# Kernel optimization log

Hardware: AMD Instinct MI355X
Metric: run time of the kernel (lower is better)

## Reference

```python
import jax, jax.numpy as jnp
import numpy as np

D_K = 512  # attn_dim

def setup_inputs() -> dict:
    key = jax.random.key(0)
    ks = jax.random.split(key, 10)
    B, S, D, A, Dv = 8, 2048, 1024, 512, 512
    Q = jax.random.normal(ks[0], (B, S, D), dtype=jnp.float32)
    K = jax.random.normal(ks[1], (B, S, D), dtype=jnp.float32)
    V = jax.random.normal(ks[2], (B, S, D), dtype=jnp.float32)
    attn_mask = jax.random.randint(ks[3], (B, S, S), 0, 2, dtype=jnp.int32)
    s = 1.0 / np.sqrt(D)
    Wq = jax.random.normal(ks[4], (A, D), dtype=jnp.float32) * s
    bq = jnp.zeros((A,), dtype=jnp.float32)
    Wk = jax.random.normal(ks[5], (A, D), dtype=jnp.float32) * s
    bk = jnp.zeros((A,), dtype=jnp.float32)
    Wv = jax.random.normal(ks[6], (Dv, D), dtype=jnp.float32) * s
    bv = jnp.zeros((Dv,), dtype=jnp.float32)
    return {"Q": Q, "K": K, "V": V, "attn_mask": attn_mask,
            "Wq": Wq, "bq": bq, "Wk": Wk, "bk": bk, "Wv": Wv, "bv": bv}

def reference(Q, K, V, attn_mask, Wq, bq, Wk, bk, Wv, bv):
    # Linear projections (torch Linear: x @ W.T + b)
    Qp = jnp.einsum('bsd,ad->bsa', Q, Wq) + bq          # [B,S,A]
    Kp = jnp.einsum('bsd,ad->bsa', K, Wk) + bk          # [B,S,A]
    WV = jnp.einsum('bsd,vd->bsv', V, Wv) + bv          # [B,S,Dv]
    scale = 1.0 / np.sqrt(D_K).astype(np.float32)
    scores = jnp.einsum('bqa,bka->bqk', Qp, Kp) * scale  # [B,S,S]
    scores = scores + attn_mask.astype(scores.dtype) * (-1e9)
    scores = jnp.swapaxes(scores, -1, -2)               # transpose BEFORE softmax
    attn = jax.nn.softmax(scores, axis=-1)              # normalize over query axis
    selfOutput = jnp.einsum('bkq,bqv->bkv', attn, WV)   # [B,S,Dv]
    return selfOutput, attn
```

## Files before the change

kernel.cpp:

```cpp
#include <hip/hip_runtime.h>
#include <stdint.h>

#define B_N   8
#define S_N   2048
#define D_N   1024
#define A_N   512
#define DV_N  512

typedef __attribute__((ext_vector_type(8))) short bf16x8;
typedef __attribute__((ext_vector_type(4))) float f32x4;

__device__ __forceinline__ unsigned short f2bf(float x) {
    union { float f; unsigned int u; } v; v.f = x;
    return (unsigned short)((v.u + 0x7fffu + ((v.u >> 16) & 1u)) >> 16);
}

__global__ void cvt_f32_bf16(const float* __restrict__ src,
                             unsigned short* __restrict__ dst, int n4) {
    int i = blockIdx.x * blockDim.x + threadIdx.x;
    if (i >= n4) return;
    float4 v = ((const float4*)src)[i];
    ushort4 o;
    o.x = f2bf(v.x); o.y = f2bf(v.y); o.z = f2bf(v.z); o.w = f2bf(v.w);
    ((ushort4*)dst)[i] = o;
}

__device__ __forceinline__ void gld_lds16(const void* g, void* l) {
    __builtin_amdgcn_global_load_lds(
        (const __attribute__((address_space(1))) unsigned int*)g,
        (__attribute__((address_space(3))) unsigned int*)l, 16, 0, 0);
}

__global__ __launch_bounds__(256) void pack_maskT(const int* __restrict__ mask,
                                                  unsigned int* __restrict__ mpT) {
    __shared__ int tile[64 * 129];
    const int b  = blockIdx.z;
    const int q0 = blockIdx.y * 64;
    const int k0 = blockIdx.x * 128;
    const int tid = threadIdx.x;
    const long long base = (long long)b * S_N * S_N;
#pragma unroll
    for (int it = 0; it < 8; ++it) {
        int c = it * 256 + tid;
        int row  = c >> 5;
        int col4 = (c & 31) * 4;
        int4 v = *(const int4*)&mask[base + (long long)(q0 + row) * S_N + k0 + col4];
        int* d = &tile[row * 129 + col4];
        d[0] = v.x; d[1] = v.y; d[2] = v.z; d[3] = v.w;
    }
    __syncthreads();
    const int wave = tid >> 6, lane = tid & 63;
#pragma unroll
    for (int kk = 0; kk < 32; ++kk) {
        const int k = wave * 32 + kk;
        const int v = tile[lane * 129 + k];
        const unsigned long long bal = __ballot(v != 0);
        if (lane == 0) {
            unsigned int* o = &mpT[(long long)(b * S_N + k0 + k) * 64 + (q0 >> 5)];
            o[0] = (unsigned int)bal;
            o[1] = (unsigned int)(bal >> 32);
        }
    }
}

template <int MODE>
__global__ __launch_bounds__(256) void gemm_nt(
    const unsigned short* __restrict__ A, const unsigned short* __restrict__ B,
    void* __restrict__ C, const float* __restrict__ bias,
    int M, int N, int K,
    long long sA, long long sB, long long sC, float scale)
{
    __shared__ __align__(16) unsigned short As[128 * 32];
    __shared__ __align__(16) unsigned short Bs[128 * 32];

    const int tid  = threadIdx.x;
    const int wave = tid >> 6;
    const int lane = tid & 63;
    const int lrow = lane & 15;
    const int quad = lane >> 4;
    const int wm = wave & 1;
    const int wn = wave >> 1;
    const int b  = blockIdx.z;
    const int m0 = blockIdx.y * 128;
    const int n0 = blockIdx.x * 128;

    const unsigned short* Ab = A + (long long)b * sA;
    const unsigned short* Bb = B + (long long)b * sB;

    f32x4 acc[4][4];
#pragma unroll
    for (int i = 0; i < 4; ++i)
#pragma unroll
        for (int j = 0; j < 4; ++j) acc[i][j] = (f32x4){0.f, 0.f, 0.f, 0.f};

    const int srow = lane >> 2;
    const int scol = (lane & 3) * 8;

    for (int kt = 0; kt < K; kt += 32) {
#pragma unroll
        for (int t = 0; t < 2; ++t) {
            const int seg = t * 4 + wave;
            const unsigned short* ga =
                Ab + (long long)(m0 + seg * 16 + srow) * K + kt + scol;
            gld_lds16(ga, &As[seg * 16 * 32]);
            const unsigned short* gb =
                Bb + (long long)(n0 + seg * 16 + srow) * K + kt + scol;
            gld_lds16(gb, &Bs[seg * 16 * 32]);
        }
        __syncthreads();

        bf16x8 af[4], bfr[4];
#pragma unroll
        for (int i = 0; i < 4; ++i)
            af[i] = *(const bf16x8*)&As[(wm * 64 + i * 16 + lrow) * 32 + quad * 8];
#pragma unroll
        for (int j = 0; j < 4; ++j)
            bfr[j] = *(const bf16x8*)&Bs[(wn * 64 + j * 16 + lrow) * 32 + quad * 8];
#pragma unroll
        for (int i = 0; i < 4; ++i)
#pragma unroll
            for (int j = 0; j < 4; ++j)
                acc[i][j] = __builtin_amdgcn_mfma_f32_16x16x32_bf16(
                    af[i], bfr[j], acc[i][j], 0, 0, 0);
        __syncthreads();
    }

#pragma unroll
    for (int i = 0; i < 4; ++i) {
        const int rowb = m0 + wm * 64 + i * 16 + quad * 4;
#pragma unroll
        for (int j = 0; j < 4; ++j) {
            const int col = n0 + wn * 64 + j * 16 + lrow;
#pragma unroll
            for (int r = 0; r < 4; ++r) {
                const int row = rowb + r;
                float v = acc[i][j][r];
                if (MODE == 0) {
                    v += bias[col];
                    ((unsigned short*)C)[(long long)row * N + col] = f2bf(v);
                } else if (MODE == 1) {
                    v += bias[row];
                    (((unsigned short*)C) + (long long)b * sC)
                        [(long long)row * N + col] = f2bf(v);
                } else if (MODE == 2) {
                    v *= scale;
                    (((float*)C) + (long long)b * sC)[(long long)row * N + col] = v;
                } else {
                    (((float*)C) + (long long)b * sC)[(long long)row * N + col] = v;
                }
            }
        }
    }
}

__global__ __launch_bounds__(256) void softmax_rows(
    float* __restrict__ sT, unsigned short* __restrict__ pbf,
    const unsigned int* __restrict__ mpT)
{
    const long long row = blockIdx.x;
    float* p = sT + row * S_N;
    unsigned short* q = pbf + row * S_N;
    const int tid = threadIdx.x;
    const int wave = tid >> 6, lane = tid & 63;

    float4 v0 = ((const float4*)p)[tid];
    float4 v1 = ((const float4*)p)[tid + 256];

    const unsigned int* mp = mpT + row * 64;
    const unsigned int w0 = mp[tid >> 3];
    const unsigned int w1 = mp[32 + (tid >> 3)];
    const int sh = (tid & 7) * 4;
    v0.x += ((w0 >> (sh + 0)) & 1u) ? -1e9f : 0.0f;
    v0.y += ((w0 >> (sh + 1)) & 1u) ? -1e9f : 0.0f;
    v0.z += ((w0 >> (sh + 2)) & 1u) ? -1e9f : 0.0f;
    v0.w += ((w0 >> (sh + 3)) & 1u) ? -1e9f : 0.0f;
    v1.x += ((w1 >> (sh + 0)) & 1u) ? -1e9f : 0.0f;
    v1.y += ((w1 >> (sh + 1)) & 1u) ? -1e9f : 0.0f;
    v1.z += ((w1 >> (sh + 2)) & 1u) ? -1e9f : 0.0f;
    v1.w += ((w1 >> (sh + 3)) & 1u) ? -1e9f : 0.0f;

    float mx = fmaxf(fmaxf(fmaxf(v0.x, v0.y), fmaxf(v0.z, v0.w)),
                     fmaxf(fmaxf(v1.x, v1.y), fmaxf(v1.z, v1.w)));
#pragma unroll
    for (int off = 32; off; off >>= 1) mx = fmaxf(mx, __shfl_xor(mx, off));

    __shared__ float redm[4];
    __shared__ float reds[4];
    if (lane == 0) redm[wave] = mx;
    __syncthreads();
    mx = fmaxf(fmaxf(redm[0], redm[1]), fmaxf(redm[2], redm[3]));

    float e[8];
    e[0] = __expf(v0.x - mx); e[1] = __expf(v0.y - mx);
    e[2] = __expf(v0.z - mx); e[3] = __expf(v0.w - mx);
    e[4] = __expf(v1.x - mx); e[5] = __expf(v1.y - mx);
    e[6] = __expf(v1.z - mx); e[7] = __expf(v1.w - mx);

    float sum = e[0] + e[1] + e[2] + e[3] + e[4] + e[5] + e[6] + e[7];
#pragma unroll
    for (int off = 32; off; off >>= 1) sum += __shfl_xor(sum, off);
    if (lane == 0) reds[wave] = sum;
    __syncthreads();
    sum = reds[0] + reds[1] + reds[2] + reds[3];
    const float inv = 1.0f / sum;

    float4 o0 = {e[0] * inv, e[1] * inv, e[2] * inv, e[3] * inv};
    float4 o1 = {e[4] * inv, e[5] * inv, e[6] * inv, e[7] * inv};
    ((float4*)p)[tid]       = o0;
    ((float4*)p)[tid + 256] = o1;
    ushort4 b0 = {f2bf(o0.x), f2bf(o0.y), f2bf(o0.z), f2bf(o0.w)};
    ushort4 b1 = {f2bf(o1.x), f2bf(o1.y), f2bf(o1.z), f2bf(o1.w)};
    ((ushort4*)q)[tid]       = b0;
    ((ushort4*)q)[tid + 256] = b1;
}

extern "C" void kernel_launch(void* const* d_in, const int* in_sizes, int n_in,
                              void* d_out, int out_size, void* d_ws, size_t ws_size,
                              hipStream_t stream) {
    const float* Q    = (const float*)d_in[0];
    const float* K    = (const float*)d_in[1];
    const float* V    = (const float*)d_in[2];
    const int*   mask = (const int*)d_in[3];
    const float* Wq   = (const float*)d_in[4];
    const float* bq   = (const float*)d_in[5];
    const float* Wk   = (const float*)d_in[6];
    const float* bk   = (const float*)d_in[7];
    const float* Wv   = (const float*)d_in[8];
    const float* bv   = (const float*)d_in[9];

    float* out      = (float*)d_out;
    float* attn_out = out + (long long)B_N * S_N * DV_N;

    unsigned short* Qbf  = (unsigned short*)d_ws;
    unsigned short* Kbf  = Qbf + (long long)B_N * S_N * D_N;
    unsigned short* attn_bf = Qbf;
    unsigned short* Vbf  = Kbf + (long long)B_N * S_N * D_N;
    unsigned short* Wqbf = Vbf + (long long)B_N * S_N * D_N;
    unsigned short* Wkbf = Wqbf + (long long)A_N * D_N;
    unsigned short* Wvbf = Wkbf + (long long)A_N * D_N;
    unsigned short* Qp   = Wvbf + (long long)DV_N * D_N;
    unsigned short* Kp   = Qp + (long long)B_N * S_N * A_N;
    unsigned short* WVt  = Kp + (long long)B_N * S_N * A_N;
    unsigned int*   mpT  = (unsigned int*)(WVt + (long long)B_N * DV_N * S_N);

    const float scale = 0.044194173824159216f;

    pack_maskT<<<dim3(S_N / 128, S_N / 64, B_N), dim3(256), 0, stream>>>(mask, mpT);

    {
        long long nQ = (long long)B_N * S_N * D_N;
        long long nW = (long long)A_N * D_N;
        int n4;
        n4 = (int)(nQ / 4);
        cvt_f32_bf16<<<dim3((n4 + 255) / 256), dim3(256), 0, stream>>>(Q, Qbf, n4);
        cvt_f32_bf16<<<dim3((n4 + 255) / 256), dim3(256), 0, stream>>>(K, Kbf, n4);
        cvt_f32_bf16<<<dim3((n4 + 255) / 256), dim3(256), 0, stream>>>(V, Vbf, n4);
        n4 = (int)(nW / 4);
        cvt_f32_bf16<<<dim3((n4 + 255) / 256), dim3(256), 0, stream>>>(Wq, Wqbf, n4);
        cvt_f32_bf16<<<dim3((n4 + 255) / 256), dim3(256), 0, stream>>>(Wk, Wkbf, n4);
        cvt_f32_bf16<<<dim3((n4 + 255) / 256), dim3(256), 0, stream>>>(Wv, Wvbf, n4);
    }

    gemm_nt<0><<<dim3(A_N / 128, (B_N * S_N) / 128, 1), dim3(256), 0, stream>>>(
        Qbf, Wqbf, (void*)Qp, bq, B_N * S_N, A_N, D_N, 0, 0, 0, 1.0f);
    gemm_nt<0><<<dim3(A_N / 128, (B_N * S_N) / 128, 1), dim3(256), 0, stream>>>(
        Kbf, Wkbf, (void*)Kp, bk, B_N * S_N, A_N, D_N, 0, 0, 0, 1.0f);
    gemm_nt<1><<<dim3(S_N / 128, DV_N / 128, B_N), dim3(256), 0, stream>>>(
        Wvbf, Vbf, (void*)WVt, bv, DV_N, S_N, D_N,
        0, (long long)S_N * D_N, (long long)DV_N * S_N, 1.0f);
    gemm_nt<2><<<dim3(S_N / 128, S_N / 128, B_N), dim3(256), 0, stream>>>(
        Kp, Qp, (void*)attn_out, nullptr, S_N, S_N, A_N,
        (long long)S_N * A_N, (long long)S_N * A_N, (long long)S_N * S_N, scale);
    softmax_rows<<<dim3(B_N * S_N), dim3(256), 0, stream>>>(attn_out, attn_bf, mpT);
    gemm_nt<3><<<dim3(DV_N / 128, S_N / 128, B_N), dim3(256), 0, stream>>>(
        attn_bf, WVt, (void*)out, nullptr, S_N, DV_N, S_N,
        (long long)S_N * S_N, (long long)DV_N * S_N, (long long)S_N * DV_N, 1.0f);
}
```

Baseline: 686.6 us.

## Fuse masked exp into score GEMM epilogue and defer softmax normalization

The score GEMM now applies scale, mask and exp in its epilogue, writes unnormalized bf16 probabilities, and accumulates per-row sums with atomics. A light normalize pass writes the fp32 attention output, and the PV GEMM divides by the row sum in its epilogue. This removes the fp32 score round-trip and the separate softmax kernel. It also merges the Q/K projections into one launch and batches the conversion kernels. Skipping max subtraction risks overflow for large scores and NaN for fully masked rows, and the atomics make row sums order-dependent.

```diff
diff --git a/kernel.cpp b/kernel.cpp
--- a/kernel.cpp
+++ b/kernel.cpp
@@ -14,15 +14,28 @@
     union { float f; unsigned int u; } v; v.f = x;
     return (unsigned short)((v.u + 0x7fffu + ((v.u >> 16) & 1u)) >> 16);
 }
-
-__global__ void cvt_f32_bf16(const float* __restrict__ src,
-                             unsigned short* __restrict__ dst, int n4) {
+__device__ __forceinline__ float bf2f(unsigned short h) {
+    union { unsigned int u; float f; } v; v.u = ((unsigned int)h) << 16;
+    return v.f;
+}
+
+__global__ void cvt3_f32_bf16(const float* __restrict__ s0, const float* __restrict__ s1,
+                              const float* __restrict__ s2,
+                              unsigned short* __restrict__ d0, unsigned short* __restrict__ d1,
+                              unsigned short* __restrict__ d2, int n4) {
+    const float* s = (blockIdx.z == 0) ? s0 : (blockIdx.z == 1) ? s1 : s2;
+    unsigned short* d = (blockIdx.z == 0) ? d0 : (blockIdx.z == 1) ? d1 : d2;
     int i = blockIdx.x * blockDim.x + threadIdx.x;
     if (i >= n4) return;
-    float4 v = ((const float4*)src)[i];
+    float4 v = ((const float4*)s)[i];
     ushort4 o;
     o.x = f2bf(v.x); o.y = f2bf(v.y); o.z = f2bf(v.z); o.w = f2bf(v.w);
-    ((ushort4*)dst)[i] = o;
+    ((ushort4*)d)[i] = o;
+}
+
+__global__ void zero_f32(float* __restrict__ p, int n) {
+    int i = blockIdx.x * blockDim.x + threadIdx.x;
+    if (i < n) p[i] = 0.0f;
 }
 
 __device__ __forceinline__ void gld_lds16(const void* g, void* l) {
@@ -66,7 +79,9 @@
 template <int MODE>
 __global__ __launch_bounds__(256) void gemm_nt(
     const unsigned short* __restrict__ A, const unsigned short* __restrict__ B,
-    void* __restrict__ C, const float* __restrict__ bias,
+    const unsigned short* __restrict__ B2,
+    void* __restrict__ C, const float* __restrict__ bias, const float* __restrict__ bias2,
+    const unsigned int* __restrict__ mpT, float* __restrict__ rowsum,
     int M, int N, int K,
     long long sA, long long sB, long long sC, float scale)
 {
@@ -85,7 +100,9 @@
     const int n0 = blockIdx.x * 128;
 
     const unsigned short* Ab = A + (long long)b * sA;
-    const unsigned short* Bb = B + (long long)b * sB;
+    const unsigned short* Bsel = (MODE == 0 && blockIdx.y >= 128) ? B2 : B;
+    const unsigned short* Bb = Bsel + (long long)b * sB;
+    const float* bias_s = (MODE == 0 && blockIdx.y >= 128) ? bias2 : bias;
 
     f32x4 acc[4][4];
 #pragma unroll
@@ -125,93 +142,89 @@
         __syncthreads();
     }
 
-#pragma unroll
-    for (int i = 0; i < 4; ++i) {
-        const int rowb = m0 + wm * 64 + i * 16 + quad * 4;
-#pragma unroll
-        for (int j = 0; j < 4; ++j) {
-            const int col = n0 + wn * 64 + j * 16 + lrow;
-#pragma unroll
-            for (int r = 0; r < 4; ++r) {
-                const int row = rowb + r;
-                float v = acc[i][j][r];
-                if (MODE == 0) {
-                    v += bias[col];
-                    ((unsigned short*)C)[(long long)row * N + col] = f2bf(v);
-                } else if (MODE == 1) {
-                    v += bias[row];
+    if (MODE == 0 || MODE == 1) {
+#pragma unroll
+        for (int i = 0; i < 4; ++i) {
+            const int rowb = m0 + wm * 64 + i * 16 + quad * 4;
+#pragma unroll
+            for (int j = 0; j < 4; ++j) {
+                const int col = n0 + wn * 64 + j * 16 + lrow;
+#pragma unroll
+                for (int r = 0; r < 4; ++r) {
+                    const int row = rowb + r;
+                    float v = acc[i][j][r];
+                    v += (MODE == 0) ? bias_s[col] : bias_s[row];
                     (((unsigned short*)C) + (long long)b * sC)
                         [(long long)row * N + col] = f2bf(v);
-                } else if (MODE == 2) {
-                    v *= scale;
-                    (((float*)C) + (long long)b * sC)[(long long)row * N + col] = v;
-                } else {
-                    (((float*)C) + (long long)b * sC)[(long long)row * N + col] = v;
                 }
             }
         }
-    }
-}
-
-__global__ __launch_bounds__(256) void softmax_rows(
-    float* __restrict__ sT, unsigned short* __restrict__ pbf,
-    const unsigned int* __restrict__ mpT)
+    } else if (MODE == 2) {
+        unsigned short* Cb = ((unsigned short*)C) + (long long)b * sC;
+        const unsigned int* mpb = mpT + ((long long)b * S_N) * 64;
+        float* rs = rowsum + (long long)b * S_N;
+#pragma unroll
+        for (int i = 0; i < 4; ++i) {
+#pragma unroll
+            for (int r = 0; r < 4; ++r) {
+                const int row = m0 + wm * 64 + i * 16 + quad * 4 + r;
+                const unsigned int* mpr = mpb + (long long)row * 64;
+                float rsum = 0.0f;
+#pragma unroll
+                for (int j = 0; j < 4; ++j) {
+                    const int col = n0 + wn * 64 + j * 16 + lrow;
+                    const float v = acc[i][j][r] * scale;
+                    const unsigned int w = mpr[col >> 5];
+                    const float e = ((w >> (col & 31)) & 1u) ? 0.0f : __expf(v);
+                    const unsigned short h = f2bf(e);
+                    Cb[(long long)row * S_N + col] = h;
+                    rsum += bf2f(h);
+                }
+                rsum += __shfl_xor(rsum, 1);
+                rsum += __shfl_xor(rsum, 2);
+                rsum += __shfl_xor(rsum, 4);
+                rsum += __shfl_xor(rsum, 8);
+                if (lrow == 0) atomicAdd(&rs[row], rsum);
+            }
+        }
+    } else {
+        float* Cb = ((float*)C) + (long long)b * sC;
+        const float* rs = rowsum + (long long)b * S_N;
+#pragma unroll
+        for (int i = 0; i < 4; ++i) {
+#pragma unroll
+            for (int r = 0; r < 4; ++r) {
+                const int row = m0 + wm * 64 + i * 16 + quad * 4 + r;
+                const float inv = 1.0f / rs[row];
+#pragma unroll
+                for (int j = 0; j < 4; ++j) {
+                    const int col = n0 + wn * 64 + j * 16 + lrow;
+                    Cb[(long long)row * N + col] = acc[i][j][r] * inv;
+                }
+            }
+        }
+    }
+}
+
+__global__ __launch_bounds__(256) void normalize_rows(
+    const unsigned short* __restrict__ ebf, const float* __restrict__ rowsum,
+    float* __restrict__ attn)
 {
     const long long row = blockIdx.x;
-    float* p = sT + row * S_N;
-    unsigned short* q = pbf + row * S_N;
+    const float inv = 1.0f / rowsum[row];
+    const ushort4* src = (const ushort4*)(ebf + row * S_N);
+    float4* dst = (float4*)(attn + row * S_N);
     const int tid = threadIdx.x;
-    const int wave = tid >> 6, lane = tid & 63;
-
-    float4 v0 = ((const float4*)p)[tid];
-    float4 v1 = ((const float4*)p)[tid + 256];
-
-    const unsigned int* mp = mpT + row * 64;
-    const unsigned int w0 = mp[tid >> 3];
-    const unsigned int w1 = mp[32 + (tid >> 3)];
-    const int sh = (tid & 7) * 4;
-    v0.x += ((w0 >> (sh + 0)) & 1u) ? -1e9f : 0.0f;
-    v0.y += ((w0 >> (sh + 1)) & 1u) ? -1e9f : 0.0f;
-    v0.z += ((w0 >> (sh + 2)) & 1u) ? -1e9f : 0.0f;
-    v0.w += ((w0 >> (sh + 3)) & 1u) ? -1e9f : 0.0f;
-    v1.x += ((w1 >> (sh + 0)) & 1u) ? -1e9f : 0.0f;
-    v1.y += ((w1 >> (sh + 1)) & 1u) ? -1e9f : 0.0f;
-    v1.z += ((w1 >> (sh + 2)) & 1u) ? -1e9f : 0.0f;
-    v1.w += ((w1 >> (sh + 3)) & 1u) ? -1e9f : 0.0f;
-
-    float mx = fmaxf(fmaxf(fmaxf(v0.x, v0.y), fmaxf(v0.z, v0.w)),
-                     fmaxf(fmaxf(v1.x, v1.y), fmaxf(v1.z, v1.w)));
-#pragma unroll
-    for (int off = 32; off; off >>= 1) mx = fmaxf(mx, __shfl_xor(mx, off));
-
-    __shared__ float redm[4];
-    __shared__ float reds[4];
-    if (lane == 0) redm[wave] = mx;
-    __syncthreads();
-    mx = fmaxf(fmaxf(redm[0], redm[1]), fmaxf(redm[2], redm[3]));
-
-    float e[8];
-    e[0] = __expf(v0.x - mx); e[1] = __expf(v0.y - mx);
-    e[2] = __expf(v0.z - mx); e[3] = __expf(v0.w - mx);
-    e[4] = __expf(v1.x - mx); e[5] = __expf(v1.y - mx);
-    e[6] = __expf(v1.z - mx); e[7] = __expf(v1.w - mx);
-
-    float sum = e[0] + e[1] + e[2] + e[3] + e[4] + e[5] + e[6] + e[7];
-#pragma unroll
-    for (int off = 32; off; off >>= 1) sum += __shfl_xor(sum, off);
-    if (lane == 0) reds[wave] = sum;
-    __syncthreads();
-    sum = reds[0] + reds[1] + reds[2] + reds[3];
-    const float inv = 1.0f / sum;
-
-    float4 o0 = {e[0] * inv, e[1] * inv, e[2] * inv, e[3] * inv};
-    float4 o1 = {e[4] * inv, e[5] * inv, e[6] * inv, e[7] * inv};
-    ((float4*)p)[tid]       = o0;
-    ((float4*)p)[tid + 256] = o1;
-    ushort4 b0 = {f2bf(o0.x), f2bf(o0.y), f2bf(o0.z), f2bf(o0.w)};
-    ushort4 b1 = {f2bf(o1.x), f2bf(o1.y), f2bf(o1.z), f2bf(o1.w)};
-    ((ushort4*)q)[tid]       = b0;
-    ((ushort4*)q)[tid + 256] = b1;
+#pragma unroll
+    for (int t = 0; t < 2; ++t) {
+        ushort4 h = src[tid + t * 256];
+        float4 o;
+        o.x = bf2f(h.x) * inv;
+        o.y = bf2f(h.y) * inv;
+        o.z = bf2f(h.z) * inv;
+        o.w = bf2f(h.w) * inv;
+        dst[tid + t * 256] = o;
+    }
 }
 
 extern "C" void kernel_launch(void* const* d_in, const int* in_sizes, int n_in,
@@ -242,37 +255,35 @@
     unsigned short* Kp   = Qp + (long long)B_N * S_N * A_N;
     unsigned short* WVt  = Kp + (long long)B_N * S_N * A_N;
     unsigned int*   mpT  = (unsigned int*)(WVt + (long long)B_N * DV_N * S_N);
+    float*          rowsum = (float*)(mpT + (long long)B_N * S_N * 64);
 
     const float scale = 0.044194173824159216f;
 
+    zero_f32<<<dim3((B_N * S_N) / 256), dim3(256), 0, stream>>>(rowsum, B_N * S_N);
     pack_maskT<<<dim3(S_N / 128, S_N / 64, B_N), dim3(256), 0, stream>>>(mask, mpT);
 
     {
-        long long nQ = (long long)B_N * S_N * D_N;
-        long long nW = (long long)A_N * D_N;
-        int n4;
-        n4 = (int)(nQ / 4);
-        cvt_f32_bf16<<<dim3((n4 + 255) / 256), dim3(256), 0, stream>>>(Q, Qbf, n4);
-        cvt_f32_bf16<<<dim3((n4 + 255) / 256), dim3(256), 0, stream>>>(K, Kbf, n4);
-        cvt_f32_bf16<<<dim3((n4 + 255) / 256), dim3(256), 0, stream>>>(V, Vbf, n4);
-        n4 = (int)(nW / 4);
-        cvt_f32_bf16<<<dim3((n4 + 255) / 256), dim3(256), 0, stream>>>(Wq, Wqbf, n4);
-        cvt_f32_bf16<<<dim3((n4 + 255) / 256), dim3(256), 0, stream>>>(Wk, Wkbf, n4);
-        cvt_f32_bf16<<<dim3((n4 + 255) / 256), dim3(256), 0, stream>>>(Wv, Wvbf, n4);
-    }
-
-    gemm_nt<0><<<dim3(A_N / 128, (B_N * S_N) / 128, 1), dim3(256), 0, stream>>>(
-        Qbf, Wqbf, (void*)Qp, bq, B_N * S_N, A_N, D_N, 0, 0, 0, 1.0f);
-    gemm_nt<0><<<dim3(A_N / 128, (B_N * S_N) / 128, 1), dim3(256), 0, stream>>>(
-        Kbf, Wkbf, (void*)Kp, bk, B_N * S_N, A_N, D_N, 0, 0, 0, 1.0f);
+        int n4 = (int)((long long)B_N * S_N * D_N / 4);
+        cvt3_f32_bf16<<<dim3((n4 + 255) / 256, 1, 3), dim3(256), 0, stream>>>(
+            Q, K, V, Qbf, Kbf, Vbf, n4);
+        int w4 = (int)((long long)A_N * D_N / 4);
+        cvt3_f32_bf16<<<dim3((w4 + 255) / 256, 1, 3), dim3(256), 0, stream>>>(
+            Wq, Wk, Wv, Wqbf, Wkbf, Wvbf, w4);
+    }
+
+    gemm_nt<0><<<dim3(A_N / 128, (2 * B_N * S_N) / 128, 1), dim3(256), 0, stream>>>(
+        Qbf, Wqbf, Wkbf, (void*)Qp, bq, bk, nullptr, nullptr,
+        2 * B_N * S_N, A_N, D_N, 0, 0, 0, 1.0f);
     gemm_nt<1><<<dim3(S_N / 128, DV_N / 128, B_N), dim3(256), 0, stream>>>(
-        Wvbf, Vbf, (void*)WVt, bv, DV_N, S_N, D_N,
-        0, (long long)S_N * D_N, (long long)DV_N * S_N, 1.0f);
+        Wvbf, Vbf, nullptr, (void*)WVt, bv, nullptr, nullptr, nullptr,
+        DV_N, S_N, D_N, 0, (long long)S_N * D_N, (long long)DV_N * S_N, 1.0f);
     gemm_nt<2><<<dim3(S_N / 128, S_N / 128, B_N), dim3(256), 0, stream>>>(
-        Kp, Qp, (void*)attn_out, nullptr, S_N, S_N, A_N,
-        (long long)S_N * A_N, (long long)S_N * A_N, (long long)S_N * S_N, scale);
-    softmax_rows<<<dim3(B_N * S_N), dim3(256), 0, stream>>>(attn_out, attn_bf, mpT);
+        Kp, Qp, nullptr, (void*)attn_bf, nullptr, nullptr, mpT, rowsum,
+        S_N, S_N, A_N, (long long)S_N * A_N, (long long)S_N * A_N,
+        (long long)S_N * S_N, scale);
+    normalize_rows<<<dim3(B_N * S_N), dim3(256), 0, stream>>>(attn_bf, rowsum, attn_out);
     gemm_nt<3><<<dim3(DV_N / 128, S_N / 128, B_N), dim3(256), 0, stream>>>(
-        attn_bf, WVt, (void*)out, nullptr, S_N, DV_N, S_N,
-        (long long)S_N * S_N, (long long)DV_N * S_N, (long long)S_N * DV_N, 1.0f);
-}
+        attn_bf, WVt, nullptr, (void*)out, nullptr, nullptr, nullptr, rowsum,
+        S_N, DV_N, S_N, (long long)S_N * S_N, (long long)DV_N * S_N,
+        (long long)S_N * DV_N, 1.0f);
+}
```

Result: no change. 677.7 us (-1.3%).
